# Kernel optimization log

Hardware: AMD Instinct MI355X
Metric: run time of the kernel (lower is better)

## Reference

```python
import jax, jax.numpy as jnp
import numpy as np

B, S, D_MODEL, H, D_FF = 2, 2048, 1024, 16, 4096
D_HEAD = D_MODEL // H
LN_EPS = 1e-5


def _xavier(key, shape):
    fan_out, fan_in = shape
    std = (2.0 / (fan_in + fan_out)) ** 0.5
    return jax.random.normal(key, shape, dtype=jnp.float32) * std


def setup_inputs() -> dict:
    key = jax.random.key(0)
    ks = jax.random.split(key, 8)
    return {
        "q": jax.random.normal(ks[0], (B, S, D_MODEL), dtype=jnp.float32),
        "k": jax.random.normal(ks[1], (B, S, D_MODEL), dtype=jnp.float32),
        "Wq": _xavier(ks[2], (D_MODEL, D_MODEL)), "bq": jnp.zeros((D_MODEL,), jnp.float32),
        "Wk": _xavier(ks[3], (D_MODEL, D_MODEL)), "bk": jnp.zeros((D_MODEL,), jnp.float32),
        "Wv": _xavier(ks[4], (D_MODEL, D_MODEL)), "bv": jnp.zeros((D_MODEL,), jnp.float32),
        "W1": _xavier(ks[5], (D_FF, D_MODEL)), "b1": jnp.zeros((D_FF,), jnp.float32),
        "W2": _xavier(ks[6], (D_MODEL, D_FF)), "b2": jnp.zeros((D_MODEL,), jnp.float32),
        "ln_g": jnp.ones((D_MODEL,), jnp.float32), "ln_b": jnp.zeros((D_MODEL,), jnp.float32),
        "use_causal_mask": 1,
    }


def _layer_norm(x, g, b):
    mu = jnp.mean(x, axis=-1, keepdims=True)
    var = jnp.mean((x - mu) ** 2, axis=-1, keepdims=True)
    return (x - mu) * jax.lax.rsqrt(var + LN_EPS) * g + b


def reference(q, k, Wq, bq, Wk, bk, Wv, bv, W1, b1, W2, b2, ln_g, ln_b, use_causal_mask):
    Bq, Sq, _ = q.shape
    Sk = k.shape[1]
    Q = q @ Wq.T + bq
    K = k @ Wk.T + bk
    V = k @ Wv.T + bv
    # [B, S, H*Dh] -> [B, H, S, Dh]
    Q_ = Q.reshape(Bq, Sq, H, D_HEAD).transpose(0, 2, 1, 3)
    K_ = K.reshape(Bq, Sk, H, D_HEAD).transpose(0, 2, 1, 3)
    V_ = V.reshape(Bq, Sk, H, D_HEAD).transpose(0, 2, 1, 3)
    scores = jnp.einsum("bhqd,bhkd->bhqk", Q_, K_) / (D_HEAD ** 0.5)
    if use_causal_mask:
        causal = jnp.tril(jnp.ones((Sq, Sk), dtype=bool))
        scores = jnp.where(causal, scores, jnp.float32(-1e9))
    sim = jax.nn.softmax(scores, axis=-1)
    att = jnp.einsum("bhqk,bhkd->bhqd", sim, V_)
    att_h = att.transpose(0, 2, 1, 3).reshape(Bq, Sq, D_MODEL)
    att_h = att_h + q                      # att_residual
    att_h = _layer_norm(att_h, ln_g, ln_b)  # att_ln (activation = identity)
    ff = jax.nn.gelu(att_h @ W1.T + b1, approximate=False) @ W2.T + b2
    return ff + att_h                      # ff_residual (no output ln / activation)
```

## Files before the change

kernel.cpp:

```cpp
#include <hip/hip_runtime.h>


typedef __bf16 bf16;
typedef float f32x4 __attribute__((ext_vector_type(4)));
typedef bf16 bf16x8 __attribute__((ext_vector_type(8)));
typedef bf16 bf16x4 __attribute__((ext_vector_type(4)));

#define LOG2E 1.44269504088896f
#define NEG_BIG (-1e30f)
#define SC_L2E  (0.125f * LOG2E)
#define SHIFT_L2 11.5415603f

__device__ __forceinline__ void async16(const void* g, void* l) {
    __builtin_amdgcn_global_load_lds((const __attribute__((address_space(1))) void*)g,
                                     (__attribute__((address_space(3))) void*)l, 16, 0, 0);
}

__global__ void detect_kernel(const unsigned* __restrict__ lng, int* __restrict__ flag)
{
    if (threadIdx.x == 0 && blockIdx.x == 0)
        *flag = (lng[0] == 0x3F803F80u) ? 1 : 0;
}

__global__ __launch_bounds__(256)
void big_cvt(const void* s0, const void* s1, const void* s2, const void* s3,
             const void* s4, const void* s5, const void* s6,
             bf16* d0, bf16* d1, bf16* d2, bf16* d3, bf16* d4, bf16* d5, bf16* d6,
             const int* __restrict__ flag)
{
    const int i = blockIdx.x * 256 + threadIdx.x;
    const void* src; bf16* dst; int loc;
    if      (i < 524288)  { src = s0; dst = d0; loc = i; }
    else if (i < 1048576) { src = s1; dst = d1; loc = i - 524288; }
    else if (i < 1179648) { src = s2; dst = d2; loc = i - 1048576; }
    else if (i < 1310720) { src = s3; dst = d3; loc = i - 1179648; }
    else if (i < 1441792) { src = s4; dst = d4; loc = i - 1310720; }
    else if (i < 1966080) { src = s5; dst = d5; loc = i - 1441792; }
    else if (i < 2490368) { src = s6; dst = d6; loc = i - 1966080; }
    else return;
    if (*flag) {
        ((bf16x8*)dst)[loc] = ((const bf16x8*)src)[loc];
    } else {
        const f32x4 a = ((const f32x4*)src)[2 * loc];
        const f32x4 b = ((const f32x4*)src)[2 * loc + 1];
        bf16x8 o;
#pragma unroll
        for (int j = 0; j < 4; ++j) { o[j] = (bf16)a[j]; o[4 + j] = (bf16)b[j]; }
        ((bf16x8*)dst)[loc] = o;
    }
}

__global__ __launch_bounds__(256)
void small_cvt(const void* s_bq, const void* s_bk, const void* s_bv,
               const void* s_b1, const void* s_b2, const void* s_lg, const void* s_lb,
               bf16* bqkv, bf16* b1, bf16* b2, bf16* lng, bf16* lnb,
               const int* __restrict__ flag)
{
    const int i = blockIdx.x * 256 + threadIdx.x;
    if (i >= 1280) return;
    const void* src; bf16* dst; int loc;
    if      (i < 128)  { src = s_bq; dst = bqkv;        loc = i; }
    else if (i < 256)  { src = s_bk; dst = bqkv + 1024; loc = i - 128; }
    else if (i < 384)  { src = s_bv; dst = bqkv + 2048; loc = i - 256; }
    else if (i < 896)  { src = s_b1; dst = b1;          loc = i - 384; }
    else if (i < 1024) { src = s_b2; dst = b2;          loc = i - 896; }
    else if (i < 1152) { src = s_lg; dst = lng;         loc = i - 1024; }
    else               { src = s_lb; dst = lnb;         loc = i - 1152; }
    if (*flag) {
        ((bf16x8*)dst)[loc] = ((const bf16x8*)src)[loc];
    } else {
        const f32x4 a = ((const f32x4*)src)[2 * loc];
        const f32x4 b = ((const f32x4*)src)[2 * loc + 1];
        bf16x8 o;
#pragma unroll
        for (int j = 0; j < 4; ++j) { o[j] = (bf16)a[j]; o[4 + j] = (bf16)b[j]; }
        ((bf16x8*)dst)[loc] = o;
    }
}

template <int EPI>
__global__ __launch_bounds__(256, 2)
void gemm_bt(const bf16* __restrict__ A, const bf16* __restrict__ A2, int nsplit,
             const bf16* __restrict__ W, const bf16* __restrict__ bias,
             bf16* __restrict__ out, int M, int N, int K)
{
    __shared__ __attribute__((aligned(16))) bf16 sA[128 * 32];
    __shared__ __attribute__((aligned(16))) bf16 sB[128 * 32];

    const int tid  = threadIdx.x;
    const int wid  = tid >> 6, lane = tid & 63;
    const int lrow = lane & 15, lgrp = lane >> 4;
    const int m0 = blockIdx.y * 128, n0 = blockIdx.x * 128;
    const int wm = (wid >> 1) * 64, wn = (wid & 1) * 64;

    const bf16* Asel = (n0 < nsplit) ? A : A2;
    const bf16* Ab = Asel + (size_t)m0 * K;
    const bf16* Wb = W + (size_t)n0 * K;

    f32x4 acc[4][4] = {};

    const int c0 = wid * 128 + lane;
    const int c1 = c0 + 64;
    const int r0 = c0 >> 2, kc0 = (c0 & 3) << 3;
    const int r1 = c1 >> 2, kc1 = (c1 & 3) << 3;

    for (int k0 = 0; k0 < K; k0 += 32) {
        async16(Ab + (size_t)r0 * K + k0 + kc0, (char*)sA + (size_t)(wid * 128) * 16);
        async16(Ab + (size_t)r1 * K + k0 + kc1, (char*)sA + (size_t)(wid * 128 + 64) * 16);
        async16(Wb + (size_t)r0 * K + k0 + kc0, (char*)sB + (size_t)(wid * 128) * 16);
        async16(Wb + (size_t)r1 * K + k0 + kc1, (char*)sB + (size_t)(wid * 128 + 64) * 16);
        __syncthreads();

        bf16x8 af[4], bfr[4];
#pragma unroll
        for (int i = 0; i < 4; ++i)
            af[i] = *(const bf16x8*)&sA[(wm + i * 16 + lrow) * 32 + lgrp * 8];
#pragma unroll
        for (int i = 0; i < 4; ++i)
            bfr[i] = *(const bf16x8*)&sB[(wn + i * 16 + lrow) * 32 + lgrp * 8];

#pragma unroll
        for (int mi = 0; mi < 4; ++mi)
#pragma unroll
            for (int ni = 0; ni < 4; ++ni)
                acc[mi][ni] = __builtin_amdgcn_mfma_f32_16x16x32_bf16(
                    af[mi], bfr[ni], acc[mi][ni], 0, 0, 0);
        __syncthreads();
    }

#pragma unroll
    for (int ni = 0; ni < 4; ++ni) {
        const int col = n0 + wn + ni * 16 + lrow;
        const float bv = (float)bias[col];
#pragma unroll
        for (int mi = 0; mi < 4; ++mi) {
            const int rowb = m0 + wm + mi * 16 + lgrp * 4;
#pragma unroll
            for (int r = 0; r < 4; ++r) {
                float v = acc[mi][ni][r] + bv;
                if (EPI == 1) v = 0.5f * v * (1.0f + erff(v * 0.70710678118654752f));
                out[(size_t)(rowb + r) * N + col] = (bf16)v;
            }
        }
    }
}

__global__ __launch_bounds__(256, 2)
void gemm64(const bf16* __restrict__ A, const bf16* __restrict__ W,
            const bf16* __restrict__ bias, const bf16* __restrict__ resid,
            void* __restrict__ outv, int M, int N, int K,
            const int* __restrict__ oflag)
{
    __shared__ __attribute__((aligned(16))) bf16 sA[64 * 32];
    __shared__ __attribute__((aligned(16))) bf16 sB[128 * 32];

    const int tid  = threadIdx.x;
    const int wid  = tid >> 6, lane = tid & 63;
    const int lrow = lane & 15, lgrp = lane >> 4;
    const int m0 = blockIdx.y * 64, n0 = blockIdx.x * 128;
    const int wm = (wid >> 1) * 32, wn = (wid & 1) * 64;

    const bf16* Ab = A + (size_t)m0 * K;
    const bf16* Wb = W + (size_t)n0 * K;

    f32x4 acc[2][4] = {};

    const int ca = wid * 64 + lane;
    const int ra = ca >> 2, ka = (ca & 3) << 3;
    const int cb0 = wid * 128 + lane, cb1 = cb0 + 64;
    const int rb0 = cb0 >> 2, kb0 = (cb0 & 3) << 3;
    const int rb1 = cb1 >> 2, kb1 = (cb1 & 3) << 3;

    for (int k0 = 0; k0 < K; k0 += 32) {
        async16(Ab + (size_t)ra * K + k0 + ka,   (char*)sA + (size_t)wid * 1024);
        async16(Wb + (size_t)rb0 * K + k0 + kb0, (char*)sB + (size_t)wid * 2048);
        async16(Wb + (size_t)rb1 * K + k0 + kb1, (char*)sB + (size_t)wid * 2048 + 1024);
        __syncthreads();

        bf16x8 af[2], bfr[4];
#pragma unroll
        for (int i = 0; i < 2; ++i)
            af[i] = *(const bf16x8*)&sA[(wm + i * 16 + lrow) * 32 + lgrp * 8];
#pragma unroll
        for (int i = 0; i < 4; ++i)
            bfr[i] = *(const bf16x8*)&sB[(wn + i * 16 + lrow) * 32 + lgrp * 8];

#pragma unroll
        for (int mi = 0; mi < 2; ++mi)
#pragma unroll
            for (int ni = 0; ni < 4; ++ni)
                acc[mi][ni] = __builtin_amdgcn_mfma_f32_16x16x32_bf16(
                    af[mi], bfr[ni], acc[mi][ni], 0, 0, 0);
        __syncthreads();
    }

    const bool out_bf16 = (*oflag != 0);
#pragma unroll
    for (int ni = 0; ni < 4; ++ni) {
        const int col = n0 + wn + ni * 16 + lrow;
        const float bv = (float)bias[col];
#pragma unroll
        for (int mi = 0; mi < 2; ++mi) {
            const int rowb = m0 + wm + mi * 16 + lgrp * 4;
#pragma unroll
            for (int r = 0; r < 4; ++r) {
                const size_t idx = (size_t)(rowb + r) * N + col;
                float v = acc[mi][ni][r] + bv + (float)resid[idx];
                if (out_bf16) ((bf16*)outv)[idx] = (bf16)v;
                else          ((float*)outv)[idx] = v;
            }
        }
    }
}

__global__ __launch_bounds__(256, 2)
void attn_kernel(const bf16* __restrict__ QKV, bf16* __restrict__ att,
                 const int* __restrict__ maskflag)
{
    __shared__ __attribute__((aligned(16))) bf16 Kl[2][64 * 64];
    __shared__ __attribute__((aligned(16))) bf16 Vt[2][64 * 72];
    __shared__ __attribute__((aligned(16))) bf16 Pl[4][32 * 68];

    const int tid  = threadIdx.x, wid = tid >> 6, lane = tid & 63;
    const int lrow = lane & 15, lgrp = lane >> 4;
    const int b = blockIdx.y >> 4, h = blockIdx.y & 15;
    const int qt = 15 - (int)blockIdx.x;
    const int q0 = qt * 128;
    const bf16* Qp = QKV + (size_t)b * 2048 * 3072 + h * 64;
    const bf16* Kp = Qp + 1024;
    const bf16* Vp = Qp + 2048;

    bf16x8 qf[2][2];
#pragma unroll
    for (int hs = 0; hs < 2; ++hs)
#pragma unroll
        for (int g = 0; g < 2; ++g)
            qf[hs][g] = *(const bf16x8*)(Qp + (size_t)(q0 + wid * 32 + hs * 16 + lrow) * 3072
                                         + g * 32 + lgrp * 8);

    f32x4 o[2][4] = {};
    float lsum[2][4] = {};

    const int causal = maskflag[0];
    const int ntiles = causal ? (2 * qt + 2) : 32;
    const int strip_lo = q0 + wid * 32;

    const int kswz = (((lane & 7) ^ ((lane >> 3) & 7)) << 3);
    auto stage_K = [&](int k0t, int buf) {
#pragma unroll
        for (int j = 0; j < 2; ++j) {
            const int blk = wid * 2 + j;
            async16(Kp + (size_t)(k0t + blk * 8 + (lane >> 3)) * 3072 + kswz,
                    (char*)&Kl[buf][0] + blk * 1024);
        }
    };

    bf16x8 va, vb;
    auto loadV = [&](int k0t) {
        const bf16* p = Vp + (size_t)(k0t + lane) * 3072 + wid * 16;
        va = *(const bf16x8*)p;
        vb = *(const bf16x8*)(p + 8);
    };
    auto scatterV = [&](int buf) {
#pragma unroll
        for (int j = 0; j < 8; ++j) Vt[buf][(wid * 16 + j) * 72 + lane] = va[j];
#pragma unroll
        for (int j = 0; j < 8; ++j) Vt[buf][(wid * 16 + 8 + j) * 72 + lane] = vb[j];
    };

    stage_K(0, 0);
    loadV(0);
    scatterV(0);
    loadV(64);

    for (int t = 0; t < ntiles; ++t) {
        const int cur = t & 1, nxt = cur ^ 1;
        const int k0 = t * 64;
        __syncthreads();
        if (t + 1 < ntiles) stage_K(k0 + 64, nxt);

        const bool active = !causal || (strip_lo + 31 >= k0);

        if (active) {
            f32x4 s[2][4];
#pragma unroll
            for (int hs = 0; hs < 2; ++hs)
#pragma unroll
                for (int n = 0; n < 4; ++n) s[hs][n] = f32x4{0.f, 0.f, 0.f, 0.f};
#pragma unroll
            for (int g = 0; g < 2; ++g)
#pragma unroll
                for (int n = 0; n < 4; ++n) {
                    bf16x8 kf = *(const bf16x8*)&Kl[cur][(n * 16 + lrow) * 64
                                                         + (((g * 4 + lgrp) ^ (lrow & 7)) << 3)];
#pragma unroll
                    for (int hs = 0; hs < 2; ++hs)
                        s[hs][n] = __builtin_amdgcn_mfma_f32_16x16x32_bf16(
                            qf[hs][g], kf, s[hs][n], 0, 0, 0);
                }

#pragma unroll
            for (int hs = 0; hs < 2; ++hs) {
                const bool need_mask = causal && (k0 + 63 > strip_lo + hs * 16);
#pragma unroll
                for (int n = 0; n < 4; ++n) {
#pragma unroll
                    for (int r = 0; r < 4; ++r) {
                        float tv = fmaf(s[hs][n][r], SC_L2E, -SHIFT_L2);
                        if (need_mask) {
                            const int gr = strip_lo + hs * 16 + lgrp * 4 + r;
                            const int gc = k0 + n * 16 + lrow;
                            if (gc > gr) tv = NEG_BIG;
                        }
                        const float p = __builtin_amdgcn_exp2f(tv);
                        s[hs][n][r] = p;
                        lsum[hs][r] += p;
                        Pl[wid][(hs * 16 + lgrp * 4 + r) * 68 + n * 16 + lrow] = (bf16)p;
                    }
                }
            }

            if (t + 1 < ntiles) {
                scatterV(nxt);
                if (t + 2 < ntiles) loadV(k0 + 128);
            }

#pragma unroll
            for (int g = 0; g < 2; ++g) {
                bf16x8 pf[2];
#pragma unroll
                for (int hs = 0; hs < 2; ++hs) {
                    const bf16* pp = &Pl[wid][(hs * 16 + lrow) * 68 + g * 32 + lgrp * 8];
                    bf16x4 lo = *(const bf16x4*)pp;
                    bf16x4 hi = *(const bf16x4*)(pp + 4);
#pragma unroll
                    for (int j = 0; j < 4; ++j) { pf[hs][j] = lo[j]; pf[hs][4 + j] = hi[j]; }
                }
#pragma unroll
                for (int n = 0; n < 4; ++n) {
                    bf16x8 vf = *(const bf16x8*)&Vt[cur][(n * 16 + lrow) * 72 + g * 32 + lgrp * 8];
#pragma unroll
                    for (int hs = 0; hs < 2; ++hs)
                        o[hs][n] = __builtin_amdgcn_mfma_f32_16x16x32_bf16(
                            pf[hs], vf, o[hs][n], 0, 0, 0);
                }
            }
        } else {
            if (t + 1 < ntiles) {
                scatterV(nxt);
                if (t + 2 < ntiles) loadV(k0 + 128);
            }
        }
    }

#pragma unroll
    for (int hs = 0; hs < 2; ++hs)
#pragma unroll
        for (int r = 0; r < 4; ++r) {
            float l = lsum[hs][r];
            for (int off = 1; off < 16; off <<= 1)
                l += __shfl_xor(l, off, 64);
            lsum[hs][r] = 1.0f / l;
        }

    const size_t ob = (size_t)b * 2048 * 1024 + h * 64;
#pragma unroll
    for (int hs = 0; hs < 2; ++hs)
#pragma unroll
        for (int r = 0; r < 4; ++r) {
            const int rowg = q0 + wid * 32 + hs * 16 + lgrp * 4 + r;
#pragma unroll
            for (int n = 0; n < 4; ++n)
                att[ob + (size_t)rowg * 1024 + n * 16 + lrow] = (bf16)(o[hs][n][r] * lsum[hs][r]);
        }
}

__global__ __launch_bounds__(256)
void ln_kernel(const bf16* __restrict__ att, const bf16* __restrict__ qin,
               const bf16* __restrict__ g, const bf16* __restrict__ bb,
               bf16* __restrict__ xout)
{
    const int row = blockIdx.x, tid = threadIdx.x;
    const int lane = tid & 63, wid = tid >> 6;

    const bf16x4 a  = ((const bf16x4*)(att + (size_t)row * 1024))[tid];
    const bf16x4 qv = ((const bf16x4*)(qin + (size_t)row * 1024))[tid];

    float v[4];
    float s = 0.f, sq = 0.f;
#pragma unroll
    for (int j = 0; j < 4; ++j) {
        v[j] = (float)a[j] + (float)qv[j];
        s += v[j];
        sq += v[j] * v[j];
    }
    for (int off = 1; off < 64; off <<= 1) {
        s  += __shfl_xor(s, off, 64);
        sq += __shfl_xor(sq, off, 64);
    }
    __shared__ float red_s[4], red_q[4];
    if (lane == 0) { red_s[wid] = s; red_q[wid] = sq; }
    __syncthreads();
    s  = red_s[0] + red_s[1] + red_s[2] + red_s[3];
    sq = red_q[0] + red_q[1] + red_q[2] + red_q[3];

    const float mean = s * (1.0f / 1024.0f);
    const float var  = sq * (1.0f / 1024.0f) - mean * mean;
    const float rstd = rsqrtf(var + 1e-5f);

    const bf16x4 gv = ((const bf16x4*)g)[tid];
    const bf16x4 bv = ((const bf16x4*)bb)[tid];
    bf16x4 ov;
#pragma unroll
    for (int j = 0; j < 4; ++j)
        ov[j] = (bf16)((v[j] - mean) * rstd * (float)gv[j] + (float)bv[j]);
    ((bf16x4*)(xout + (size_t)row * 1024))[tid] = ov;
}

extern "C" void kernel_launch(void* const* d_in, const int* in_sizes, int n_in,
                              void* d_out, int out_size, void* d_ws, size_t ws_size,
                              hipStream_t stream)
{
    (void)in_sizes; (void)n_in; (void)out_size; (void)ws_size;

    const void* q_raw  = d_in[0];
    const void* k_raw  = d_in[1];
    const void* Wq_raw = d_in[2];
    const void* bq_raw = d_in[3];
    const void* Wk_raw = d_in[4];
    const void* bk_raw = d_in[5];
    const void* Wv_raw = d_in[6];
    const void* bv_raw = d_in[7];
    const void* W1_raw = d_in[8];
    const void* b1_raw = d_in[9];
    const void* W2_raw = d_in[10];
    const void* b2_raw = d_in[11];
    const void* lng_raw = d_in[12];
    const void* lnb_raw = d_in[13];
    const int*  mask   = (const int*)d_in[14];

    char* ws = (char*)d_ws;
    const size_t MB = (size_t)1 << 20;
    const size_t KB = (size_t)1 << 10;
    bf16* qc    = (bf16*)(ws);
    bf16* kc    = (bf16*)(ws + 8 * MB);
    bf16* Wqkvc = (bf16*)(ws + 16 * MB);
    bf16* W1c   = (bf16*)(ws + 22 * MB);
    bf16* W2c   = (bf16*)(ws + 30 * MB);
    bf16* bqkvc = (bf16*)(ws + 38 * MB);
    bf16* b1c   = (bf16*)(ws + 38 * MB + 8  * KB);
    bf16* b2c   = (bf16*)(ws + 38 * MB + 16 * KB);
    bf16* lngc  = (bf16*)(ws + 38 * MB + 24 * KB);
    bf16* lnbc  = (bf16*)(ws + 38 * MB + 32 * KB);
    int*  flag  = (int*) (ws + 38 * MB + 40 * KB);
    bf16* QKVb  = (bf16*)(ws + 38 * MB + 256 * KB);
    bf16* attb  = (bf16*)(ws + 62 * MB + 256 * KB);
    bf16* xb    = (bf16*)(ws + 70 * MB + 256 * KB);
    bf16* hb    = (bf16*)(ws + 38 * MB + 256 * KB);

    dim3 blk(256);
    detect_kernel<<<1, 64, 0, stream>>>((const unsigned*)lng_raw, flag);

    big_cvt<<<9728, blk, 0, stream>>>(q_raw, k_raw, Wq_raw, Wk_raw, Wv_raw, W1_raw, W2_raw,
                                      qc, kc, Wqkvc, Wqkvc + 1024 * 1024,
                                      Wqkvc + 2048 * 1024, W1c, W2c, flag);
    small_cvt<<<5, blk, 0, stream>>>(bq_raw, bk_raw, bv_raw, b1_raw, b2_raw,
                                     lng_raw, lnb_raw,
                                     bqkvc, b1c, b2c, lngc, lnbc, flag);

    gemm_bt<0><<<dim3(24, 32), blk, 0, stream>>>(qc, kc, 1024, Wqkvc, bqkvc,
                                                 QKVb, 4096, 3072, 1024);
    attn_kernel<<<dim3(16, 32), blk, 0, stream>>>(QKVb, attb, mask);
    ln_kernel<<<dim3(4096), blk, 0, stream>>>(attb, qc, lngc, lnbc, xb);
    gemm_bt<1><<<dim3(32, 32), blk, 0, stream>>>(xb, xb, 1 << 30, W1c, b1c,
                                                 hb, 4096, 4096, 1024);
    gemm64<<<dim3(8, 64), blk, 0, stream>>>(hb, W2c, b2c, xb, d_out,
                                            4096, 1024, 4096, flag);
}
```

Baseline: 368.3 us.

## Deepen GEMM K-tile with swizzled LDS and software-pipeline attention PV step

In gemm64 the K step per iteration grows from 32 to 64. Global-to-LDS loads are XOR-swizzled so each loop iteration issues two MFMA sub-steps per barrier pair, halving the number of barriers, and the swizzle is meant to avoid LDS bank conflicts. In the attention kernel, the P·V MFMAs for tile t-1 are deferred to the start of iteration t. P is double-buffered and V triple-buffered so that product can overlap with the QK^T and softmax of the next tile. The cost is more LDS per block (about 78 KB), which could limit the two-blocks-per-CU target, and a more complex buffer-index schedule.

Result: no change. 372.0 us (+1.0%).

```diff
diff --git a/kernel.cpp b/kernel.cpp
--- a/kernel.cpp
+++ b/kernel.cpp
@@ -151,8 +151,8 @@
             void* __restrict__ outv, int M, int N, int K,
             const int* __restrict__ oflag)
 {
-    __shared__ __attribute__((aligned(16))) bf16 sA[64 * 32];
-    __shared__ __attribute__((aligned(16))) bf16 sB[128 * 32];
+    __shared__ __attribute__((aligned(16))) bf16 sA[64 * 64];
+    __shared__ __attribute__((aligned(16))) bf16 sB[128 * 64];
 
     const int tid  = threadIdx.x;
     const int wid  = tid >> 6, lane = tid & 63;
@@ -165,32 +165,50 @@
 
     f32x4 acc[2][4] = {};
 
-    const int ca = wid * 64 + lane;
-    const int ra = ca >> 2, ka = (ca & 3) << 3;
-    const int cb0 = wid * 128 + lane, cb1 = cb0 + 64;
-    const int rb0 = cb0 >> 2, kb0 = (cb0 & 3) << 3;
-    const int rb1 = cb1 >> 2, kb1 = (cb1 & 3) << 3;
-
-    for (int k0 = 0; k0 < K; k0 += 32) {
-        async16(Ab + (size_t)ra * K + k0 + ka,   (char*)sA + (size_t)wid * 1024);
-        async16(Wb + (size_t)rb0 * K + k0 + kb0, (char*)sB + (size_t)wid * 2048);
-        async16(Wb + (size_t)rb1 * K + k0 + kb1, (char*)sB + (size_t)wid * 2048 + 1024);
+    int arow[2], asrc[2];
+#pragma unroll
+    for (int j = 0; j < 2; ++j) {
+        const int c = wid * 128 + j * 64 + lane;
+        arow[j] = c >> 3;
+        asrc[j] = (((c & 7) ^ ((c >> 3) & 7)) << 3);
+    }
+    int brow[4], bsrc[4];
+#pragma unroll
+    for (int j = 0; j < 4; ++j) {
+        const int c = wid * 256 + j * 64 + lane;
+        brow[j] = c >> 3;
+        bsrc[j] = (((c & 7) ^ ((c >> 3) & 7)) << 3);
+    }
+
+    for (int k0 = 0; k0 < K; k0 += 64) {
+#pragma unroll
+        for (int j = 0; j < 2; ++j)
+            async16(Ab + (size_t)arow[j] * K + k0 + asrc[j],
+                    (char*)sA + (size_t)(wid * 128 + j * 64) * 16);
+#pragma unroll
+        for (int j = 0; j < 4; ++j)
+            async16(Wb + (size_t)brow[j] * K + k0 + bsrc[j],
+                    (char*)sB + (size_t)(wid * 256 + j * 64) * 16);
         __syncthreads();
 
-        bf16x8 af[2], bfr[4];
-#pragma unroll
-        for (int i = 0; i < 2; ++i)
-            af[i] = *(const bf16x8*)&sA[(wm + i * 16 + lrow) * 32 + lgrp * 8];
-#pragma unroll
-        for (int i = 0; i < 4; ++i)
-            bfr[i] = *(const bf16x8*)&sB[(wn + i * 16 + lrow) * 32 + lgrp * 8];
-
-#pragma unroll
-        for (int mi = 0; mi < 2; ++mi)
-#pragma unroll
-            for (int ni = 0; ni < 4; ++ni)
-                acc[mi][ni] = __builtin_amdgcn_mfma_f32_16x16x32_bf16(
-                    af[mi], bfr[ni], acc[mi][ni], 0, 0, 0);
+#pragma unroll
+        for (int ks = 0; ks < 2; ++ks) {
+            const int swz = ((ks * 4 + lgrp) ^ (lrow & 7)) << 3;
+            bf16x8 af[2], bfr[4];
+#pragma unroll
+            for (int i = 0; i < 2; ++i)
+                af[i] = *(const bf16x8*)&sA[(wm + i * 16 + lrow) * 64 + swz];
+#pragma unroll
+            for (int i = 0; i < 4; ++i)
+                bfr[i] = *(const bf16x8*)&sB[(wn + i * 16 + lrow) * 64 + swz];
+
+#pragma unroll
+            for (int mi = 0; mi < 2; ++mi)
+#pragma unroll
+                for (int ni = 0; ni < 4; ++ni)
+                    acc[mi][ni] = __builtin_amdgcn_mfma_f32_16x16x32_bf16(
+                        af[mi], bfr[ni], acc[mi][ni], 0, 0, 0);
+        }
         __syncthreads();
     }
 
@@ -218,8 +236,8 @@
                  const int* __restrict__ maskflag)
 {
     __shared__ __attribute__((aligned(16))) bf16 Kl[2][64 * 64];
-    __shared__ __attribute__((aligned(16))) bf16 Vt[2][64 * 72];
-    __shared__ __attribute__((aligned(16))) bf16 Pl[4][32 * 68];
+    __shared__ __attribute__((aligned(16))) bf16 Vt[3][64 * 72];
+    __shared__ __attribute__((aligned(16))) bf16 Pl[4][2][32 * 68];
 
     const int tid  = threadIdx.x, wid = tid >> 6, lane = tid & 63;
     const int lrow = lane & 15, lgrp = lane >> 4;
@@ -268,16 +286,43 @@
         for (int j = 0; j < 8; ++j) Vt[buf][(wid * 16 + 8 + j) * 72 + lane] = vb[j];
     };
 
+    auto do_PV = [&](int pb, int vb3) {
+#pragma unroll
+        for (int g = 0; g < 2; ++g) {
+            bf16x8 pf[2];
+#pragma unroll
+            for (int hs = 0; hs < 2; ++hs) {
+                const bf16* pp = &Pl[wid][pb][(hs * 16 + lrow) * 68 + g * 32 + lgrp * 8];
+                bf16x4 lo = *(const bf16x4*)pp;
+                bf16x4 hi = *(const bf16x4*)(pp + 4);
+#pragma unroll
+                for (int j = 0; j < 4; ++j) { pf[hs][j] = lo[j]; pf[hs][4 + j] = hi[j]; }
+            }
+#pragma unroll
+            for (int n = 0; n < 4; ++n) {
+                bf16x8 vf = *(const bf16x8*)&Vt[vb3][(n * 16 + lrow) * 72 + g * 32 + lgrp * 8];
+#pragma unroll
+                for (int hs = 0; hs < 2; ++hs)
+                    o[hs][n] = __builtin_amdgcn_mfma_f32_16x16x32_bf16(
+                        pf[hs], vf, o[hs][n], 0, 0, 0);
+            }
+        }
+    };
+
     stage_K(0, 0);
     loadV(0);
     scatterV(0);
     loadV(64);
 
+    bool prev_active = false;
+
     for (int t = 0; t < ntiles; ++t) {
-        const int cur = t & 1, nxt = cur ^ 1;
         const int k0 = t * 64;
+
+        if (prev_active) do_PV((t - 1) & 1, (t + 2) % 3);
+
         __syncthreads();
-        if (t + 1 < ntiles) stage_K(k0 + 64, nxt);
+        if (t + 1 < ntiles) stage_K(k0 + 64, (t + 1) & 1);
 
         const bool active = !causal || (strip_lo + 31 >= k0);
 
@@ -291,8 +336,8 @@
             for (int g = 0; g < 2; ++g)
 #pragma unroll
                 for (int n = 0; n < 4; ++n) {
-                    bf16x8 kf = *(const bf16x8*)&Kl[cur][(n * 16 + lrow) * 64
-                                                         + (((g * 4 + lgrp) ^ (lrow & 7)) << 3)];
+                    bf16x8 kf = *(const bf16x8*)&Kl[t & 1][(n * 16 + lrow) * 64
+                                                           + (((g * 4 + lgrp) ^ (lrow & 7)) << 3)];
 #pragma unroll
                     for (int hs = 0; hs < 2; ++hs)
                         s[hs][n] = __builtin_amdgcn_mfma_f32_16x16x32_bf16(
@@ -315,43 +360,21 @@
                         const float p = __builtin_amdgcn_exp2f(tv);
                         s[hs][n][r] = p;
                         lsum[hs][r] += p;
-                        Pl[wid][(hs * 16 + lgrp * 4 + r) * 68 + n * 16 + lrow] = (bf16)p;
+                        Pl[wid][t & 1][(hs * 16 + lgrp * 4 + r) * 68 + n * 16 + lrow] = (bf16)p;
                     }
                 }
             }
-
-            if (t + 1 < ntiles) {
-                scatterV(nxt);
-                if (t + 2 < ntiles) loadV(k0 + 128);
-            }
-
-#pragma unroll
-            for (int g = 0; g < 2; ++g) {
-                bf16x8 pf[2];
-#pragma unroll
-                for (int hs = 0; hs < 2; ++hs) {
-                    const bf16* pp = &Pl[wid][(hs * 16 + lrow) * 68 + g * 32 + lgrp * 8];
-                    bf16x4 lo = *(const bf16x4*)pp;
-                    bf16x4 hi = *(const bf16x4*)(pp + 4);
-#pragma unroll
-                    for (int j = 0; j < 4; ++j) { pf[hs][j] = lo[j]; pf[hs][4 + j] = hi[j]; }
-                }
-#pragma unroll
-                for (int n = 0; n < 4; ++n) {
-                    bf16x8 vf = *(const bf16x8*)&Vt[cur][(n * 16 + lrow) * 72 + g * 32 + lgrp * 8];
-#pragma unroll
-                    for (int hs = 0; hs < 2; ++hs)
-                        o[hs][n] = __builtin_amdgcn_mfma_f32_16x16x32_bf16(
-                            pf[hs], vf, o[hs][n], 0, 0, 0);
-                }
-            }
-        } else {
-            if (t + 1 < ntiles) {
-                scatterV(nxt);
-                if (t + 2 < ntiles) loadV(k0 + 128);
-            }
-        }
-    }
+        }
+
+        if (t + 1 < ntiles) {
+            scatterV((t + 1) % 3);
+            if (t + 2 < ntiles) loadV(k0 + 128);
+        }
+
+        prev_active = active;
+    }
+
+    if (prev_active) do_PV((ntiles - 1) & 1, (ntiles - 1) % 3);
 
 #pragma unroll
     for (int hs = 0; hs < 2; ++hs)
```
